# Optimization experiments

Hardware: AMD Instinct MI355X
Metric: run time of the kernel (lower is better)

Reference implementation:

```python
import jax, jax.numpy as jnp
import numpy as np

D_MODEL = 1024
EXPAND = 2
D_INNER = D_MODEL * EXPAND  # 2048
D_STATE = 16
FFN_HIDDEN = ((D_MODEL * 4 * 2 // 3) + 63) // 64 * 64  # 2752
EPS = 1e-6


def rmsnorm(x, w):
    return x * jax.lax.rsqrt(jnp.mean(x * x, axis=-1, keepdims=True) + EPS) * w


def selective_scan(z, dt_w, dt_b, x_proj_w, A_log, Dp):
    # z: [B, L, d_inner]
    dt = jax.nn.softplus(jnp.einsum('bld,ed->ble', z, dt_w) + dt_b)     # [B,L,d]
    BC = jnp.einsum('bld,nd->bln', z, x_proj_w)                          # [B,L,2n]
    Bm, Cm = BC[..., :D_STATE], BC[..., D_STATE:]                        # [B,L,n]
    A = -jnp.exp(A_log)                                                  # [d,n]
    dA = jnp.exp(dt[..., None] * A)                                      # [B,L,d,n]
    dBz = (dt * z)[..., None] * Bm[:, :, None, :]                        # [B,L,d,n]

    def combine(e1, e2):
        a1, b1 = e1
        a2, b2 = e2
        return (a1 * a2, a2 * b1 + b2)

    _, h = jax.lax.associative_scan(combine, (dA, dBz), axis=1)          # [B,L,d,n]
    y = jnp.einsum('bldn,bln->bld', h, Cm) + z * Dp
    return y


def setup_inputs() -> dict:
    key = jax.random.key(0)
    ks = jax.random.split(key, 12)
    s = 0.02
    inp = {
        'x': jax.random.normal(ks[0], (2, 1024, D_MODEL), dtype=jnp.float32),
        'norm1_w': jnp.ones((D_MODEL,), jnp.float32),
        'in_proj_w': jax.random.normal(ks[1], (D_INNER, D_MODEL), jnp.float32) * s,
        'gate_proj_w': jax.random.normal(ks[2], (D_INNER, D_MODEL), jnp.float32) * s,
        'dt_w': jax.random.normal(ks[3], (D_INNER, D_INNER), jnp.float32) * s,
        'dt_b': jnp.full((D_INNER,), -2.0, jnp.float32),
        'x_proj_w': jax.random.normal(ks[4], (2 * D_STATE, D_INNER), jnp.float32) * s,
        'A_log': jnp.broadcast_to(jnp.log(jnp.arange(1, D_STATE + 1, dtype=jnp.float32)), (D_INNER, D_STATE)).copy(),
        'Dp': jnp.ones((D_INNER,), jnp.float32),
        'out_proj_w': jax.random.normal(ks[5], (D_MODEL, D_INNER), jnp.float32) * s,
        'ffn_norm_w': jnp.ones((D_MODEL,), jnp.float32),
        'ffn_gate_w': jax.random.normal(ks[6], (FFN_HIDDEN, D_MODEL), jnp.float32) * s,
        'ffn_up_w': jax.random.normal(ks[7], (FFN_HIDDEN, D_MODEL), jnp.float32) * s,
        'ffn_down_w': jax.random.normal(ks[8], (D_MODEL, FFN_HIDDEN), jnp.float32) * s,
    }
    return inp


def reference(x, norm1_w, in_proj_w, gate_proj_w, dt_w, dt_b, x_proj_w, A_log, Dp,
              out_proj_w, ffn_norm_w, ffn_gate_w, ffn_up_w, ffn_down_w):
    residual = x
    h = rmsnorm(x, norm1_w)
    z = jnp.einsum('bld,ed->ble', h, in_proj_w)
    gate = jax.nn.sigmoid(jnp.einsum('bld,ed->ble', h, gate_proj_w))
    z = z * gate
    ssm_out = selective_scan(z, dt_w, dt_b, x_proj_w, A_log, Dp)
    x = residual + jnp.einsum('ble,de->bld', ssm_out, out_proj_w)
    hn = rmsnorm(x, ffn_norm_w)
    ff = jnp.einsum('blh,dh->bld',
                    jax.nn.silu(jnp.einsum('bld,hd->blh', hn, ffn_gate_w)) *
                    jnp.einsum('bld,hd->blh', hn, ffn_up_w),
                    ffn_down_w)
    return x + ff
```

## Files before the change

### kernel.cpp

```cpp
#include <hip/hip_runtime.h>
#include <cstdint>
#include <cstddef>


#define BM 128
#define BN 128
#define BK 32

typedef __attribute__((ext_vector_type(8))) short short8;
typedef __attribute__((ext_vector_type(4))) float floatx4;

__device__ __forceinline__ unsigned short f2bf(float f) {
  unsigned int u = __builtin_bit_cast(unsigned int, f);
  u = u + 0x7fffu + ((u >> 16) & 1u);
  return (unsigned short)(u >> 16);
}
__device__ __forceinline__ float bf2f(unsigned short u) {
  return __builtin_bit_cast(float, (unsigned int)u << 16);
}

__device__ __forceinline__ void async_copy16(const unsigned short* g, unsigned short* l) {
  __builtin_amdgcn_global_load_lds(
      (__attribute__((address_space(1))) void*)(const_cast<unsigned short*>(g)),
      (__attribute__((address_space(3))) void*)(l), 16, 0, 0);
}

struct CvtArgs {
  const float* src[8];
  unsigned short* dst[8];
  int rows[8];
  int cols4[8];
  int g0[9];
};

__global__ __launch_bounds__(256) void cvt_all(
    CvtArgs a, int nCvt,
    const float* __restrict__ x, const float* __restrict__ nw,
    unsigned short* __restrict__ h_bf) {
  __shared__ float ws_[4];
  if ((int)blockIdx.x >= nCvt) {
    int row = blockIdx.x - nCvt, t = threadIdx.x;
    float4 v = *(const float4*)&x[(size_t)row * 1024 + t * 4];
    float ss = v.x * v.x + v.y * v.y + v.z * v.z + v.w * v.w;
#pragma unroll
    for (int m = 1; m < 64; m <<= 1) ss += __shfl_xor(ss, m);
    if ((t & 63) == 0) ws_[t >> 6] = ss;
    __syncthreads();
    float tot = ws_[0] + ws_[1] + ws_[2] + ws_[3];
    float scale = rsqrtf(tot * (1.0f / 1024.0f) + 1e-6f);
    ushort4 o;
    o.x = f2bf(v.x * scale * nw[t * 4 + 0]);
    o.y = f2bf(v.y * scale * nw[t * 4 + 1]);
    o.z = f2bf(v.z * scale * nw[t * 4 + 2]);
    o.w = f2bf(v.w * scale * nw[t * 4 + 3]);
    *(ushort4*)&h_bf[(size_t)row * 1024 + t * 4] = o;
    return;
  }
  int i = blockIdx.x * 256 + threadIdx.x;
  if (i >= a.g0[8]) return;
  int s = 0;
#pragma unroll
  for (int k = 1; k < 8; ++k) s += (i >= a.g0[k]) ? 1 : 0;
  int li = i - a.g0[s];
  int cols4 = a.cols4[s];
  int r = li / cols4, c = li - r * cols4;
  ushort4 o = {0, 0, 0, 0};
  if (r < a.rows[s]) {
    float4 v = *(const float4*)&a.src[s][((size_t)r * cols4 + c) * 4];
    o.x = f2bf(v.x); o.y = f2bf(v.y); o.z = f2bf(v.z); o.w = f2bf(v.w);
  }
  *(ushort4*)&a.dst[s][((size_t)r * cols4 + c) * 4] = o;
}

__global__ __launch_bounds__(256) void rmsnorm_fuse3(
    const float* __restrict__ x, const float* __restrict__ p,
    const float* __restrict__ w,
    float* __restrict__ x2, unsigned short* __restrict__ outbf) {
  int row = blockIdx.x, t = threadIdx.x;
  size_t off = (size_t)row * 1024 + t * 4;
  float4 a = *(const float4*)&x[off];
  float4 b = *(const float4*)&p[off];
  float4 c = *(const float4*)&p[2097152ull + off];
  float4 d = *(const float4*)&p[4194304ull + off];
  float4 e = *(const float4*)&p[6291456ull + off];
  float4 v = {a.x + b.x + c.x + d.x + e.x, a.y + b.y + c.y + d.y + e.y,
              a.z + b.z + c.z + d.z + e.z, a.w + b.w + c.w + d.w + e.w};
  *(float4*)&x2[off] = v;
  float ss = v.x * v.x + v.y * v.y + v.z * v.z + v.w * v.w;
#pragma unroll
  for (int m = 1; m < 64; m <<= 1) ss += __shfl_xor(ss, m);
  __shared__ float ws_[4];
  if ((t & 63) == 0) ws_[t >> 6] = ss;
  __syncthreads();
  float tot = ws_[0] + ws_[1] + ws_[2] + ws_[3];
  float scale = rsqrtf(tot * (1.0f / 1024.0f) + 1e-6f);
  ushort4 o;
  o.x = f2bf(v.x * scale * w[t * 4 + 0]);
  o.y = f2bf(v.y * scale * w[t * 4 + 1]);
  o.z = f2bf(v.z * scale * w[t * 4 + 2]);
  o.w = f2bf(v.w * scale * w[t * 4 + 3]);
  *(ushort4*)&outbf[off] = o;
}

__global__ void final_add(const float* __restrict__ x2, const float* __restrict__ p,
                          float* __restrict__ out) {
  int i = blockIdx.x * 256 + threadIdx.x;
  float4 a = ((const float4*)x2)[i];
  float4 b = ((const float4*)p)[i];
  float4 c = ((const float4*)(p + 2097152ull))[i];
  float4 d = ((const float4*)(p + 4194304ull))[i];
  float4 e = ((const float4*)(p + 6291456ull))[i];
  float4 o = {a.x + b.x + c.x + d.x + e.x, a.y + b.y + c.y + d.y + e.y,
              a.z + b.z + c.z + d.z + e.z, a.w + b.w + c.w + d.w + e.w};
  ((float4*)out)[i] = o;
}

__global__ __launch_bounds__(256) void dtbc_red(
    const float* __restrict__ pd, const float* __restrict__ pb,
    const float* __restrict__ dtb, float* __restrict__ dt32,
    float* __restrict__ bc128) {
  int bi = blockIdx.x, t = threadIdx.x;
  if (bi < 4096) {
    int i = bi * 256 + t;
    int c4 = i & 511;
    size_t off = (size_t)i * 4;
    float4 a = *(const float4*)&pd[off];
    float4 b = *(const float4*)&pd[4194304ull + off];
    float4 g = *(const float4*)&dtb[c4 * 4];
    float4 v = {a.x + b.x + g.x, a.y + b.y + g.y, a.z + b.z + g.z, a.w + b.w + g.w};
    float4 o;
    o.x = fmaxf(v.x, 0.0f) + log1pf(__expf(-fabsf(v.x)));
    o.y = fmaxf(v.y, 0.0f) + log1pf(__expf(-fabsf(v.y)));
    o.z = fmaxf(v.z, 0.0f) + log1pf(__expf(-fabsf(v.z)));
    o.w = fmaxf(v.w, 0.0f) + log1pf(__expf(-fabsf(v.w)));
    *(float4*)&dt32[off] = o;
  } else {
    int i = (bi - 4096) * 256 + t;
    size_t off = (size_t)i * 4;
    float4 a = *(const float4*)&pb[off];
    float4 b = *(const float4*)&pb[262144ull + off];
    float4 o = {a.x + b.x, a.y + b.y, a.z + b.z, a.w + b.w};
    *(float4*)&bc128[off] = o;
  }
}

template <int EPI, int MAP>
__global__ __launch_bounds__(256, 4) void gemm_bt(
    const unsigned short* __restrict__ A,
    const unsigned short* __restrict__ W1,
    const unsigned short* __restrict__ W2,
    int n1_blocks, int ncols, int K,
    void* __restrict__ Cv, int ldc,
    float* __restrict__ C2) {
  __shared__ __align__(16) unsigned short As[2][BM * BK];
  __shared__ __align__(16) unsigned short Bs[2][BN * BK];
  int bn, bm, ks = 0, k0 = 0, nk;
  if (MAP == 0) {
    bn = blockIdx.x; bm = blockIdx.y;
    nk = K / BK;
  } else if (MAP == 2) {
    int l = blockIdx.x, i = l >> 3;
    bn = (l & 7) + 8 * (i % 6);
    bm = i / 6;
    if (bn >= ncols) return;
    nk = K / BK;
  } else if (MAP == 3) {
    bn = blockIdx.x & 7; bm = blockIdx.y;
    ks = blockIdx.x >> 3;
    int nkt = K / BK, base = nkt >> 2, rem = nkt & 3;
    nk = base + (ks < rem ? 1 : 0);
    int k0t = ks * base + (ks < rem ? ks : rem);
    k0 = k0t * BK;
  } else {
    if ((int)blockIdx.y < gridDim.y - 1) { bn = blockIdx.x; bm = blockIdx.y; }
    else                                 { bn = n1_blocks;  bm = blockIdx.x; }
    ks = blockIdx.z;
    k0 = ks * (K >> 1);
    nk = (K >> 1) / BK;
  }
  const int tid = threadIdx.x;
  const int wave = tid >> 6, lane = tid & 63;
  const unsigned short* W;
  int wrow0;
  if (bn < n1_blocks) { W = W1; wrow0 = bn * BN; }
  else                { W = W2; wrow0 = (bn - n1_blocks) * BN; }
  const int m0 = bm * BM;
  const int wm = wave >> 1, wn = wave & 1;
  const int l15 = lane & 15, quad = lane >> 4;

  floatx4 acc[4][4] = {};

  const int c0 = wave * 64 + lane;
  const int r0 = c0 >> 2, k0off = ((c0 & 3) ^ ((r0 >> 1) & 3)) * 8;
  const int c1 = c0 + 256;
  const int r1 = c1 >> 2, k1off = ((c1 & 3) ^ ((r1 >> 1) & 3)) * 8;

  auto stage = [&](int kb, int buf) {
    async_copy16(A + (size_t)(m0 + r0) * K + kb + k0off, &As[buf][c0 * 8]);
    async_copy16(A + (size_t)(m0 + r1) * K + kb + k1off, &As[buf][c1 * 8]);
    async_copy16(W + (size_t)(wrow0 + r0) * K + kb + k0off, &Bs[buf][c0 * 8]);
    async_copy16(W + (size_t)(wrow0 + r1) * K + kb + k1off, &Bs[buf][c1 * 8]);
  };

  stage(k0, 0);
  for (int kt = 0; kt < nk; ++kt) {
    const int cur = kt & 1;
    __syncthreads();
    if (kt + 1 < nk) stage(k0 + (kt + 1) * BK, cur ^ 1);

    short8 af[4], bf4[4];
#pragma unroll
    for (int i = 0; i < 4; ++i) {
      int row = wm * 64 + i * 16 + l15;
      af[i] = *(const short8*)&As[cur][(row * 4 + (quad ^ ((row >> 1) & 3))) * 8];
    }
#pragma unroll
    for (int j = 0; j < 4; ++j) {
      int row = wn * 64 + j * 16 + l15;
      bf4[j] = *(const short8*)&Bs[cur][(row * 4 + (quad ^ ((row >> 1) & 3))) * 8];
    }
#pragma unroll
    for (int i = 0; i < 4; ++i)
#pragma unroll
      for (int j = 0; j < 4; ++j)
        acc[i][j] = __builtin_amdgcn_mfma_f32_16x16x32_bf16(af[i], bf4[j], acc[i][j], 0, 0, 0);
  }

#pragma unroll
  for (int i = 0; i < 4; ++i)
#pragma unroll
    for (int j = 0; j < 4; ++j)
#pragma unroll
      for (int r = 0; r < 4; ++r) {
        int gr = m0 + wm * 64 + i * 16 + quad * 4 + r;
        int lc = wn * 64 + j * 16 + l15;
        int gc = bn * BN + lc;
        float v = acc[i][j][r];
        if (EPI == 0) {
          ((unsigned short*)Cv)[(size_t)gr * ldc + gc] = f2bf(v);
        } else if (EPI == 3) {
          ((float*)Cv)[(size_t)ks * 2097152 + (size_t)gr * ldc + gc] = v;
        } else {
          if (bn < n1_blocks)
            ((float*)Cv)[(size_t)ks * 4194304 + (size_t)gr * ldc + gc] = v;
          else
            C2[(size_t)ks * 262144 + (size_t)gr * 128 + lc] = v;
        }
      }
}

__global__ void zfuse(const unsigned short* __restrict__ zg, float* __restrict__ z32,
                      unsigned short* __restrict__ zbf) {
  int i = blockIdx.x * blockDim.x + threadIdx.x;
  int row = i >> 9, c4 = i & 511;
  ushort4 zr4 = *(const ushort4*)&zg[(size_t)row * 4096 + c4 * 4];
  ushort4 gr4 = *(const ushort4*)&zg[(size_t)row * 4096 + 2048 + c4 * 4];
  float4 o;
  o.x = bf2f(zr4.x) / (1.0f + __expf(-bf2f(gr4.x)));
  o.y = bf2f(zr4.y) / (1.0f + __expf(-bf2f(gr4.y)));
  o.z = bf2f(zr4.z) / (1.0f + __expf(-bf2f(gr4.z)));
  o.w = bf2f(zr4.w) / (1.0f + __expf(-bf2f(gr4.w)));
  *(float4*)&z32[(size_t)row * 2048 + c4 * 4] = o;
  ushort4 ob;
  ob.x = f2bf(o.x); ob.y = f2bf(o.y); ob.z = f2bf(o.z); ob.w = f2bf(o.w);
  *(ushort4*)&zbf[(size_t)row * 2048 + c4 * 4] = ob;
}

__device__ __forceinline__ void stage_bc(const float* __restrict__ bc128,
                                         int b, int c, float* bcs, int tid) {
  int row = tid >> 3, c4 = tid & 7;
  const float* src = bc128 + ((size_t)b * 1024 + c * 32 + row) * 128 + c4 * 4;
  *(float4*)&bcs[row * 32 + c4 * 4] = *(const float4*)src;
}

__global__ __launch_bounds__(256) void scan_phase1(
    const float* __restrict__ dt, const float* __restrict__ z,
    const float* __restrict__ bc128, const float* __restrict__ A_log,
    float* __restrict__ P, float* __restrict__ S) {
  const int d = blockIdx.x * 256 + threadIdx.x;
  const int c = blockIdx.y, b = blockIdx.z;
  __shared__ float bcs[1024];
  stage_bc(bc128, b, c, bcs, threadIdx.x);
  __syncthreads();
  float A2[16];
#pragma unroll
  for (int n = 0; n < 16; ++n) A2[n] = -__expf(A_log[d * 16 + n]) * 1.44269504f;
  float p[16], s[16];
#pragma unroll
  for (int n = 0; n < 16; ++n) { p[n] = 1.0f; s[n] = 0.0f; }
  const size_t base = ((size_t)b * 1024 + c * 32) * 2048 + d;
#pragma unroll 4
  for (int t = 0; t < 32; ++t) {
    float dtv = dt[base + (size_t)t * 2048];
    float zv  = z [base + (size_t)t * 2048];
    float dtz = dtv * zv;
#pragma unroll
    for (int n = 0; n < 16; ++n) {
      float dA = exp2f(dtv * A2[n]);
      s[n] = __builtin_fmaf(dA, s[n], dtz * bcs[t * 32 + n]);
      p[n] *= dA;
    }
  }
  float* Pp = P + (((size_t)c * 2 + b) * 2048 + d) * 16;
  float* Sp = S + (((size_t)c * 2 + b) * 2048 + d) * 16;
#pragma unroll
  for (int n = 0; n < 16; ++n) { Pp[n] = p[n]; Sp[n] = s[n]; }
}

__global__ __launch_bounds__(256) void scan_phase2(
    const float* __restrict__ P, const float* __restrict__ S,
    float* __restrict__ H) {
  int i = blockIdx.x * 256 + threadIdx.x;
  float h = 0.0f;
#pragma unroll
  for (int c = 0; c < 32; ++c) {
    size_t idx = (size_t)c * 65536 + i;
    H[idx] = h;
    h = __builtin_fmaf(P[idx], h, S[idx]);
  }
}

__global__ __launch_bounds__(256) void scan_phase3(
    const float* __restrict__ dt, const float* __restrict__ z,
    const float* __restrict__ bc128, const float* __restrict__ A_log,
    const float* __restrict__ Dp, const float* __restrict__ H,
    unsigned short* __restrict__ ybf) {
  const int d = blockIdx.x * 256 + threadIdx.x;
  const int c = blockIdx.y, b = blockIdx.z;
  __shared__ float bcs[1024];
  stage_bc(bc128, b, c, bcs, threadIdx.x);
  __syncthreads();
  float A2[16];
#pragma unroll
  for (int n = 0; n < 16; ++n) A2[n] = -__expf(A_log[d * 16 + n]) * 1.44269504f;
  float h[16];
  const float* Hp = H + (((size_t)c * 2 + b) * 2048 + d) * 16;
#pragma unroll
  for (int n = 0; n < 16; ++n) h[n] = Hp[n];
  const float Dd = Dp[d];
  const size_t base = ((size_t)b * 1024 + c * 32) * 2048 + d;
#pragma unroll 4
  for (int t = 0; t < 32; ++t) {
    float dtv = dt[base + (size_t)t * 2048];
    float zv  = z [base + (size_t)t * 2048];
    float dtz = dtv * zv;
    float y = zv * Dd;
#pragma unroll
    for (int n = 0; n < 16; ++n) {
      float dA = exp2f(dtv * A2[n]);
      h[n] = __builtin_fmaf(dA, h[n], dtz * bcs[t * 32 + n]);
      y = __builtin_fmaf(h[n], bcs[t * 32 + 16 + n], y);
    }
    ybf[base + (size_t)t * 2048] = f2bf(y);
  }
}

__global__ void actfuse(const unsigned short* __restrict__ gu,
                        unsigned short* __restrict__ act) {
  int i = blockIdx.x * blockDim.x + threadIdx.x;
  int row = i / 688, c4 = i - row * 688;
  ushort4 g4 = *(const ushort4*)&gu[(size_t)row * 5632 + c4 * 4];
  ushort4 u4 = *(const ushort4*)&gu[(size_t)row * 5632 + 2816 + c4 * 4];
  float gx = bf2f(g4.x), gy = bf2f(g4.y), gz = bf2f(g4.z), gw = bf2f(g4.w);
  ushort4 o;
  o.x = f2bf(gx / (1.0f + __expf(-gx)) * bf2f(u4.x));
  o.y = f2bf(gy / (1.0f + __expf(-gy)) * bf2f(u4.y));
  o.z = f2bf(gz / (1.0f + __expf(-gz)) * bf2f(u4.z));
  o.w = f2bf(gw / (1.0f + __expf(-gw)) * bf2f(u4.w));
  *(ushort4*)&act[(size_t)row * 2752 + c4 * 4] = o;
}

extern "C" void kernel_launch(void* const* d_in, const int* in_sizes, int n_in,
                              void* d_out, int out_size, void* d_ws, size_t ws_size,
                              hipStream_t stream) {
  const float* x         = (const float*)d_in[0];
  const float* norm1_w   = (const float*)d_in[1];
  const float* in_proj_w = (const float*)d_in[2];
  const float* gate_w    = (const float*)d_in[3];
  const float* dt_w      = (const float*)d_in[4];
  const float* dt_b      = (const float*)d_in[5];
  const float* x_proj_w  = (const float*)d_in[6];
  const float* A_log     = (const float*)d_in[7];
  const float* Dp        = (const float*)d_in[8];
  const float* out_w     = (const float*)d_in[9];
  const float* ffn_nw    = (const float*)d_in[10];
  const float* ffn_g     = (const float*)d_in[11];
  const float* ffn_u     = (const float*)d_in[12];
  const float* ffn_d     = (const float*)d_in[13];
  float* out = (float*)d_out;

  char* p = (char*)d_ws;
  auto alloc = [&](size_t b) { char* r = p; p += (b + 255) & ~(size_t)255; return r; };
  unsigned short* h_bf   = (unsigned short*)alloc(2048ull * 1024 * 2);
  float* big             = (float*)alloc(2048ull * 5632 * 4);
  float* pk              = (float*)alloc(4ull * 2048 * 1024 * 4);
  float* pkb             = (float*)alloc(2ull * 2048 * 128 * 4);
  float* z32             = (float*)alloc(2048ull * 2048 * 4);
  unsigned short* zbf    = (unsigned short*)alloc(2048ull * 2048 * 2);
  float* dt32            = (float*)alloc(2048ull * 2048 * 4);
  float* bc128           = (float*)alloc(2048ull * 128 * 4);
  unsigned short* ybf    = (unsigned short*)alloc(2048ull * 2048 * 2);
  float* x2              = (float*)alloc(2048ull * 1024 * 4);
  unsigned short* hn_bf  = (unsigned short*)alloc(2048ull * 1024 * 2);
  unsigned short* act_bf = (unsigned short*)alloc(2048ull * 2752 * 2);
  unsigned short* w_in   = (unsigned short*)alloc(2048ull * 1024 * 2);
  unsigned short* w_gate = (unsigned short*)alloc(2048ull * 1024 * 2);
  unsigned short* w_dt   = (unsigned short*)alloc(2048ull * 2048 * 2);
  unsigned short* w_xp   = (unsigned short*)alloc(128ull * 2048 * 2);
  unsigned short* w_out  = (unsigned short*)alloc(1024ull * 2048 * 2);
  unsigned short* w_g    = (unsigned short*)alloc(2816ull * 1024 * 2);
  unsigned short* w_u    = (unsigned short*)alloc(2816ull * 1024 * 2);
  unsigned short* w_d    = (unsigned short*)alloc(1024ull * 2752 * 2);

  unsigned short* zg_bf = (unsigned short*)big;
  unsigned short* gu_bf = (unsigned short*)big;
  float* pkd = big;
  float* Pb = big;
  float* Sb = big + 2097152;
  float* Hb = big + 4194304;

  CvtArgs ca;
  ca.src[0] = in_proj_w; ca.dst[0] = w_in;   ca.rows[0] = 2048; ca.cols4[0] = 256;
  ca.src[1] = gate_w;    ca.dst[1] = w_gate; ca.rows[1] = 2048; ca.cols4[1] = 256;
  ca.src[2] = dt_w;      ca.dst[2] = w_dt;   ca.rows[2] = 2048; ca.cols4[2] = 512;
  ca.src[3] = x_proj_w;  ca.dst[3] = w_xp;   ca.rows[3] = 32;   ca.cols4[3] = 512;
  ca.src[4] = out_w;     ca.dst[4] = w_out;  ca.rows[4] = 1024; ca.cols4[4] = 512;
  ca.src[5] = ffn_g;     ca.dst[5] = w_g;    ca.rows[5] = 2752; ca.cols4[5] = 256;
  ca.src[6] = ffn_u;     ca.dst[6] = w_u;    ca.rows[6] = 2752; ca.cols4[6] = 256;
  ca.src[7] = ffn_d;     ca.dst[7] = w_d;    ca.rows[7] = 1024; ca.cols4[7] = 688;
  int dstrows[8] = {2048, 2048, 2048, 128, 1024, 2816, 2816, 1024};
  int acc_g = 0;
  for (int s = 0; s < 8; ++s) { ca.g0[s] = acc_g; acc_g += dstrows[s] * ca.cols4[s]; }
  ca.g0[8] = acc_g;
  int nCvt = (acc_g + 255) / 256;
  cvt_all<<<nCvt + 2048, 256, 0, stream>>>(ca, nCvt, x, norm1_w, h_bf);

  gemm_bt<0, 0><<<dim3(32, 16), 256, 0, stream>>>(h_bf, w_in, w_gate, 16, 0, 1024, zg_bf, 4096, nullptr);
  zfuse<<<4096, 256, 0, stream>>>(zg_bf, z32, zbf);
  gemm_bt<4, 4><<<dim3(16, 17, 2), 256, 0, stream>>>(zbf, w_dt, w_xp, 16, 0, 2048, pkd, 2048, pkb);
  dtbc_red<<<4352, 256, 0, stream>>>(pkd, pkb, dt_b, dt32, bc128);
  scan_phase1<<<dim3(8, 32, 2), 256, 0, stream>>>(dt32, z32, bc128, A_log, Pb, Sb);
  scan_phase2<<<256, 256, 0, stream>>>(Pb, Sb, Hb);
  scan_phase3<<<dim3(8, 32, 2), 256, 0, stream>>>(dt32, z32, bc128, A_log, Dp, Hb, ybf);
  gemm_bt<3, 3><<<dim3(32, 16), 256, 0, stream>>>(ybf, w_out, w_out, 8, 0, 2048, pk, 1024, nullptr);
  rmsnorm_fuse3<<<2048, 256, 0, stream>>>(x, pk, ffn_nw, x2, hn_bf);
  gemm_bt<0, 2><<<768, 256, 0, stream>>>(hn_bf, w_g, w_u, 22, 44, 1024, gu_bf, 5632, nullptr);
  actfuse<<<5504, 256, 0, stream>>>(gu_bf, act_bf);
  gemm_bt<3, 3><<<dim3(32, 16), 256, 0, stream>>>(act_bf, w_d, w_d, 8, 0, 2752, pk, 1024, nullptr);
  final_add<<<2048, 256, 0, stream>>>(x2, pk, out);
}
```

Before: 396.8 us.

## Fuse gating and SwiGLU into GEMM epilogues via interleaved weights; fold dt reduction into scan

```diff
diff --git a/kernel.cpp b/kernel.cpp
--- a/kernel.cpp
+++ b/kernel.cpp
@@ -15,9 +15,6 @@
   u = u + 0x7fffu + ((u >> 16) & 1u);
   return (unsigned short)(u >> 16);
 }
-__device__ __forceinline__ float bf2f(unsigned short u) {
-  return __builtin_bit_cast(float, (unsigned int)u << 16);
-}
 
 __device__ __forceinline__ void async_copy16(const unsigned short* g, unsigned short* l) {
   __builtin_amdgcn_global_load_lds(
@@ -25,13 +22,8 @@
       (__attribute__((address_space(3))) void*)(l), 16, 0, 0);
 }
 
-struct CvtArgs {
-  const float* src[8];
-  unsigned short* dst[8];
-  int rows[8];
-  int cols4[8];
-  int g0[9];
-};
+struct Seg { const float* src; unsigned short* dst; int mode; int aux; };
+struct CvtArgs { Seg sg[10]; int g0[11]; };
 
 __global__ __launch_bounds__(256) void cvt_all(
     CvtArgs a, int nCvt,
@@ -57,19 +49,25 @@
     return;
   }
   int i = blockIdx.x * 256 + threadIdx.x;
-  if (i >= a.g0[8]) return;
+  if (i >= a.g0[10]) return;
   int s = 0;
 #pragma unroll
-  for (int k = 1; k < 8; ++k) s += (i >= a.g0[k]) ? 1 : 0;
+  for (int k = 1; k < 10; ++k) s += (i >= a.g0[k]) ? 1 : 0;
   int li = i - a.g0[s];
-  int cols4 = a.cols4[s];
-  int r = li / cols4, c = li - r * cols4;
-  ushort4 o = {0, 0, 0, 0};
-  if (r < a.rows[s]) {
-    float4 v = *(const float4*)&a.src[s][((size_t)r * cols4 + c) * 4];
-    o.x = f2bf(v.x); o.y = f2bf(v.y); o.z = f2bf(v.z); o.w = f2bf(v.w);
-  }
-  *(ushort4*)&a.dst[s][((size_t)r * cols4 + c) * 4] = o;
+  Seg sg = a.sg[s];
+  if (sg.mode == 2) {
+    ushort4 z = {0, 0, 0, 0};
+    *(ushort4*)&sg.dst[(size_t)li * 4] = z;
+  } else if (sg.mode == 0) {
+    float4 v = *(const float4*)&sg.src[(size_t)li * 4];
+    ushort4 o = {f2bf(v.x), f2bf(v.y), f2bf(v.z), f2bf(v.w)};
+    *(ushort4*)&sg.dst[(size_t)li * 4] = o;
+  } else {
+    int r = li >> 8, c = li & 255;
+    float4 v = *(const float4*)&sg.src[(size_t)li * 4];
+    ushort4 o = {f2bf(v.x), f2bf(v.y), f2bf(v.z), f2bf(v.w)};
+    *(ushort4*)&sg.dst[((size_t)(2 * r + sg.aux) * 256 + c) * 4] = o;
+  }
 }
 
 __global__ __launch_bounds__(256) void rmsnorm_fuse3(
@@ -113,35 +111,6 @@
   float4 o = {a.x + b.x + c.x + d.x + e.x, a.y + b.y + c.y + d.y + e.y,
               a.z + b.z + c.z + d.z + e.z, a.w + b.w + c.w + d.w + e.w};
   ((float4*)out)[i] = o;
-}
-
-__global__ __launch_bounds__(256) void dtbc_red(
-    const float* __restrict__ pd, const float* __restrict__ pb,
-    const float* __restrict__ dtb, float* __restrict__ dt32,
-    float* __restrict__ bc128) {
-  int bi = blockIdx.x, t = threadIdx.x;
-  if (bi < 4096) {
-    int i = bi * 256 + t;
-    int c4 = i & 511;
-    size_t off = (size_t)i * 4;
-    float4 a = *(const float4*)&pd[off];
-    float4 b = *(const float4*)&pd[4194304ull + off];
-    float4 g = *(const float4*)&dtb[c4 * 4];
-    float4 v = {a.x + b.x + g.x, a.y + b.y + g.y, a.z + b.z + g.z, a.w + b.w + g.w};
-    float4 o;
-    o.x = fmaxf(v.x, 0.0f) + log1pf(__expf(-fabsf(v.x)));
-    o.y = fmaxf(v.y, 0.0f) + log1pf(__expf(-fabsf(v.y)));
-    o.z = fmaxf(v.z, 0.0f) + log1pf(__expf(-fabsf(v.z)));
-    o.w = fmaxf(v.w, 0.0f) + log1pf(__expf(-fabsf(v.w)));
-    *(float4*)&dt32[off] = o;
-  } else {
-    int i = (bi - 4096) * 256 + t;
-    size_t off = (size_t)i * 4;
-    float4 a = *(const float4*)&pb[off];
-    float4 b = *(const float4*)&pb[262144ull + off];
-    float4 o = {a.x + b.x, a.y + b.y, a.z + b.z, a.w + b.w};
-    *(float4*)&bc128[off] = o;
-  }
 }
 
 template <int EPI, int MAP>
@@ -236,63 +205,71 @@
         int lc = wn * 64 + j * 16 + l15;
         int gc = bn * BN + lc;
         float v = acc[i][j][r];
-        if (EPI == 0) {
-          ((unsigned short*)Cv)[(size_t)gr * ldc + gc] = f2bf(v);
-        } else if (EPI == 3) {
+        if (EPI == 3) {
           ((float*)Cv)[(size_t)ks * 2097152 + (size_t)gr * ldc + gc] = v;
-        } else {
+        } else if (EPI == 4) {
           if (bn < n1_blocks)
             ((float*)Cv)[(size_t)ks * 4194304 + (size_t)gr * ldc + gc] = v;
           else
             C2[(size_t)ks * 262144 + (size_t)gr * 128 + lc] = v;
+        } else if (EPI == 5) {
+          float other = __shfl_xor(v, 1);
+          if (!(l15 & 1)) {
+            float zv = v / (1.0f + __expf(-other));
+            int f = gc >> 1;
+            ((float*)Cv)[(size_t)gr * 2048 + f] = zv;
+            ((unsigned short*)C2)[(size_t)gr * 2048 + f] = f2bf(zv);
+          }
+        } else {
+          float other = __shfl_xor(v, 1);
+          if (!(l15 & 1)) {
+            int f = gc >> 1;
+            if (f < 2752) {
+              float av = v / (1.0f + __expf(-v)) * other;
+              ((unsigned short*)Cv)[(size_t)gr * 2752 + f] = f2bf(av);
+            }
+          }
         }
       }
 }
 
-__global__ void zfuse(const unsigned short* __restrict__ zg, float* __restrict__ z32,
-                      unsigned short* __restrict__ zbf) {
-  int i = blockIdx.x * blockDim.x + threadIdx.x;
-  int row = i >> 9, c4 = i & 511;
-  ushort4 zr4 = *(const ushort4*)&zg[(size_t)row * 4096 + c4 * 4];
-  ushort4 gr4 = *(const ushort4*)&zg[(size_t)row * 4096 + 2048 + c4 * 4];
-  float4 o;
-  o.x = bf2f(zr4.x) / (1.0f + __expf(-bf2f(gr4.x)));
-  o.y = bf2f(zr4.y) / (1.0f + __expf(-bf2f(gr4.y)));
-  o.z = bf2f(zr4.z) / (1.0f + __expf(-bf2f(gr4.z)));
-  o.w = bf2f(zr4.w) / (1.0f + __expf(-bf2f(gr4.w)));
-  *(float4*)&z32[(size_t)row * 2048 + c4 * 4] = o;
-  ushort4 ob;
-  ob.x = f2bf(o.x); ob.y = f2bf(o.y); ob.z = f2bf(o.z); ob.w = f2bf(o.w);
-  *(ushort4*)&zbf[(size_t)row * 2048 + c4 * 4] = ob;
-}
-
-__device__ __forceinline__ void stage_bc(const float* __restrict__ bc128,
-                                         int b, int c, float* bcs, int tid) {
+__device__ __forceinline__ void stage_bc2(const float* __restrict__ pb,
+                                          int b, int c, float* bcs, int tid) {
   int row = tid >> 3, c4 = tid & 7;
-  const float* src = bc128 + ((size_t)b * 1024 + c * 32 + row) * 128 + c4 * 4;
-  *(float4*)&bcs[row * 32 + c4 * 4] = *(const float4*)src;
+  size_t idx = ((size_t)b * 1024 + c * 32 + row) * 128 + c4 * 4;
+  float4 aa = *(const float4*)&pb[idx];
+  float4 bb = *(const float4*)&pb[262144ull + idx];
+  float4 sm = {aa.x + bb.x, aa.y + bb.y, aa.z + bb.z, aa.w + bb.w};
+  *(float4*)&bcs[row * 32 + c4 * 4] = sm;
+}
+
+__device__ __forceinline__ float softplus_f(float v) {
+  return fmaxf(v, 0.0f) + log1pf(__expf(-fabsf(v)));
 }
 
 __global__ __launch_bounds__(256) void scan_phase1(
-    const float* __restrict__ dt, const float* __restrict__ z,
-    const float* __restrict__ bc128, const float* __restrict__ A_log,
+    const float* __restrict__ pd, const float* __restrict__ pb,
+    const float* __restrict__ dtb, const float* __restrict__ z,
+    const float* __restrict__ A_log,
     float* __restrict__ P, float* __restrict__ S) {
   const int d = blockIdx.x * 256 + threadIdx.x;
   const int c = blockIdx.y, b = blockIdx.z;
   __shared__ float bcs[1024];
-  stage_bc(bc128, b, c, bcs, threadIdx.x);
+  stage_bc2(pb, b, c, bcs, threadIdx.x);
   __syncthreads();
   float A2[16];
 #pragma unroll
   for (int n = 0; n < 16; ++n) A2[n] = -__expf(A_log[d * 16 + n]) * 1.44269504f;
+  const float bias = dtb[d];
   float p[16], s[16];
 #pragma unroll
   for (int n = 0; n < 16; ++n) { p[n] = 1.0f; s[n] = 0.0f; }
   const size_t base = ((size_t)b * 1024 + c * 32) * 2048 + d;
 #pragma unroll 4
   for (int t = 0; t < 32; ++t) {
-    float dtv = dt[base + (size_t)t * 2048];
-    float zv  = z [base + (size_t)t * 2048];
+    size_t off = base + (size_t)t * 2048;
+    float dtv = softplus_f(pd[off] + pd[4194304ull + off] + bias);
+    float zv  = z[off];
     float dtz = dtv * zv;
 #pragma unroll
     for (int n = 0; n < 16; ++n) {
@@ -321,18 +298,19 @@
 }
 
 __global__ __launch_bounds__(256) void scan_phase3(
-    const float* __restrict__ dt, const float* __restrict__ z,
-    const float* __restrict__ bc128, const float* __restrict__ A_log,
-    const float* __restrict__ Dp, const float* __restrict__ H,
-    unsigned short* __restrict__ ybf) {
+    const float* __restrict__ pd, const float* __restrict__ pb,
+    const float* __restrict__ dtb, const float* __restrict__ z,
+    const float* __restrict__ A_log, const float* __restrict__ Dp,
+    const float* __restrict__ H, unsigned short* __restrict__ ybf) {
   const int d = blockIdx.x * 256 + threadIdx.x;
   const int c = blockIdx.y, b = blockIdx.z;
   __shared__ float bcs[1024];
-  stage_bc(bc128, b, c, bcs, threadIdx.x);
+  stage_bc2(pb, b, c, bcs, threadIdx.x);
   __syncthreads();
   float A2[16];
 #pragma unroll
   for (int n = 0; n < 16; ++n) A2[n] = -__expf(A_log[d * 16 + n]) * 1.44269504f;
+  const float bias = dtb[d];
   float h[16];
   const float* Hp = H + (((size_t)c * 2 + b) * 2048 + d) * 16;
 #pragma unroll
@@ -341,8 +319,9 @@
   const size_t base = ((size_t)b * 1024 + c * 32) * 2048 + d;
 #pragma unroll 4
   for (int t = 0; t < 32; ++t) {
-    float dtv = dt[base + (size_t)t * 2048];
-    float zv  = z [base + (size_t)t * 2048];
+    size_t off = base + (size_t)t * 2048;
+    float dtv = softplus_f(pd[off] + pd[4194304ull + off] + bias);
+    float zv  = z[off];
     float dtz = dtv * zv;
     float y = zv * Dd;
 #pragma unroll
@@ -351,23 +330,8 @@
       h[n] = __builtin_fmaf(dA, h[n], dtz * bcs[t * 32 + n]);
       y = __builtin_fmaf(h[n], bcs[t * 32 + 16 + n], y);
     }
-    ybf[base + (size_t)t * 2048] = f2bf(y);
-  }
-}
-
-__global__ void actfuse(const unsigned short* __restrict__ gu,
-                        unsigned short* __restrict__ act) {
-  int i = blockIdx.x * blockDim.x + threadIdx.x;
-  int row = i / 688, c4 = i - row * 688;
-  ushort4 g4 = *(const ushort4*)&gu[(size_t)row * 5632 + c4 * 4];
-  ushort4 u4 = *(const ushort4*)&gu[(size_t)row * 5632 + 2816 + c4 * 4];
-  float gx = bf2f(g4.x), gy = bf2f(g4.y), gz = bf2f(g4.z), gw = bf2f(g4.w);
-  ushort4 o;
-  o.x = f2bf(gx / (1.0f + __expf(-gx)) * bf2f(u4.x));
-  o.y = f2bf(gy / (1.0f + __expf(-gy)) * bf2f(u4.y));
-  o.z = f2bf(gz / (1.0f + __expf(-gz)) * bf2f(u4.z));
-  o.w = f2bf(gw / (1.0f + __expf(-gw)) * bf2f(u4.w));
-  *(ushort4*)&act[(size_t)row * 2752 + c4 * 4] = o;
+    ybf[off] = f2bf(y);
+  }
 }
 
 extern "C" void kernel_launch(void* const* d_in, const int* in_sizes, int n_in,
@@ -397,55 +361,52 @@
   float* pkb             = (float*)alloc(2ull * 2048 * 128 * 4);
   float* z32             = (float*)alloc(2048ull * 2048 * 4);
   unsigned short* zbf    = (unsigned short*)alloc(2048ull * 2048 * 2);
-  float* dt32            = (float*)alloc(2048ull * 2048 * 4);
-  float* bc128           = (float*)alloc(2048ull * 128 * 4);
   unsigned short* ybf    = (unsigned short*)alloc(2048ull * 2048 * 2);
   float* x2              = (float*)alloc(2048ull * 1024 * 4);
   unsigned short* hn_bf  = (unsigned short*)alloc(2048ull * 1024 * 2);
   unsigned short* act_bf = (unsigned short*)alloc(2048ull * 2752 * 2);
-  unsigned short* w_in   = (unsigned short*)alloc(2048ull * 1024 * 2);
-  unsigned short* w_gate = (unsigned short*)alloc(2048ull * 1024 * 2);
+  unsigned short* w_zg   = (unsigned short*)alloc(4096ull * 1024 * 2);
   unsigned short* w_dt   = (unsigned short*)alloc(2048ull * 2048 * 2);
   unsigned short* w_xp   = (unsigned short*)alloc(128ull * 2048 * 2);
   unsigned short* w_out  = (unsigned short*)alloc(1024ull * 2048 * 2);
-  unsigned short* w_g    = (unsigned short*)alloc(2816ull * 1024 * 2);
-  unsigned short* w_u    = (unsigned short*)alloc(2816ull * 1024 * 2);
+  unsigned short* w_gu   = (unsigned short*)alloc(5632ull * 1024 * 2);
   unsigned short* w_d    = (unsigned short*)alloc(1024ull * 2752 * 2);
 
-  unsigned short* zg_bf = (unsigned short*)big;
-  unsigned short* gu_bf = (unsigned short*)big;
   float* pkd = big;
-  float* Pb = big;
-  float* Sb = big + 2097152;
-  float* Hb = big + 4194304;
+  float* Pb = pk;
+  float* Sb = pk + 2097152;
+  float* Hb = pk + 4194304;
 
   CvtArgs ca;
-  ca.src[0] = in_proj_w; ca.dst[0] = w_in;   ca.rows[0] = 2048; ca.cols4[0] = 256;
-  ca.src[1] = gate_w;    ca.dst[1] = w_gate; ca.rows[1] = 2048; ca.cols4[1] = 256;
-  ca.src[2] = dt_w;      ca.dst[2] = w_dt;   ca.rows[2] = 2048; ca.cols4[2] = 512;
-  ca.src[3] = x_proj_w;  ca.dst[3] = w_xp;   ca.rows[3] = 32;   ca.cols4[3] = 512;
-  ca.src[4] = out_w;     ca.dst[4] = w_out;  ca.rows[4] = 1024; ca.cols4[4] = 512;
-  ca.src[5] = ffn_g;     ca.dst[5] = w_g;    ca.rows[5] = 2752; ca.cols4[5] = 256;
-  ca.src[6] = ffn_u;     ca.dst[6] = w_u;    ca.rows[6] = 2752; ca.cols4[6] = 256;
-  ca.src[7] = ffn_d;     ca.dst[7] = w_d;    ca.rows[7] = 1024; ca.cols4[7] = 688;
-  int dstrows[8] = {2048, 2048, 2048, 128, 1024, 2816, 2816, 1024};
+  auto seg = [&](int idx, const float* s, unsigned short* d, int mode, int aux, int groups,
+                 int& acc_g) {
+    ca.sg[idx] = {s, d, mode, aux};
+    ca.g0[idx] = acc_g;
+    acc_g += groups;
+  };
   int acc_g = 0;
-  for (int s = 0; s < 8; ++s) { ca.g0[s] = acc_g; acc_g += dstrows[s] * ca.cols4[s]; }
-  ca.g0[8] = acc_g;
+  seg(0, in_proj_w, w_zg,                 1, 0, 2048 * 256, acc_g);
+  seg(1, gate_w,    w_zg,                 1, 1, 2048 * 256, acc_g);
+  seg(2, dt_w,      w_dt,                 0, 0, 2048 * 512, acc_g);
+  seg(3, x_proj_w,  w_xp,                 0, 0, 32 * 512,   acc_g);
+  seg(4, nullptr,   w_xp + 32ull * 2048,  2, 0, 96 * 512,   acc_g);
+  seg(5, out_w,     w_out,                0, 0, 1024 * 512, acc_g);
+  seg(6, ffn_g,     w_gu,                 1, 0, 2752 * 256, acc_g);
+  seg(7, ffn_u,     w_gu,                 1, 1, 2752 * 256, acc_g);
+  seg(8, nullptr,   w_gu + 5504ull * 1024, 2, 0, 128 * 256, acc_g);
+  seg(9, ffn_d,     w_d,                  0, 0, 1024 * 688, acc_g);
+  ca.g0[10] = acc_g;
   int nCvt = (acc_g + 255) / 256;
   cvt_all<<<nCvt + 2048, 256, 0, stream>>>(ca, nCvt, x, norm1_w, h_bf);
 
-  gemm_bt<0, 0><<<dim3(32, 16), 256, 0, stream>>>(h_bf, w_in, w_gate, 16, 0, 1024, zg_bf, 4096, nullptr);
-  zfuse<<<4096, 256, 0, stream>>>(zg_bf, z32, zbf);
+  gemm_bt<5, 0><<<dim3(32, 16), 256, 0, stream>>>(h_bf, w_zg, w_zg, 32, 0, 1024, z32, 2048, (float*)zbf);
   gemm_bt<4, 4><<<dim3(16, 17, 2), 256, 0, stream>>>(zbf, w_dt, w_xp, 16, 0, 2048, pkd, 2048, pkb);
-  dtbc_red<<<4352, 256, 0, stream>>>(pkd, pkb, dt_b, dt32, bc128);
-  scan_phase1<<<dim3(8, 32, 2), 256, 0, stream>>>(dt32, z32, bc128, A_log, Pb, Sb);
+  scan_phase1<<<dim3(8, 32, 2), 256, 0, stream>>>(pkd, pkb, dt_b, z32, A_log, Pb, Sb);
   scan_phase2<<<256, 256, 0, stream>>>(Pb, Sb, Hb);
-  scan_phase3<<<dim3(8, 32, 2), 256, 0, stream>>>(dt32, z32, bc128, A_log, Dp, Hb, ybf);
+  scan_phase3<<<dim3(8, 32, 2), 256, 0, stream>>>(pkd, pkb, dt_b, z32, A_log, Dp, Hb, ybf);
   gemm_bt<3, 3><<<dim3(32, 16), 256, 0, stream>>>(ybf, w_out, w_out, 8, 0, 2048, pk, 1024, nullptr);
   rmsnorm_fuse3<<<2048, 256, 0, stream>>>(x, pk, ffn_nw, x2, hn_bf);
-  gemm_bt<0, 2><<<768, 256, 0, stream>>>(hn_bf, w_g, w_u, 22, 44, 1024, gu_bf, 5632, nullptr);
-  actfuse<<<5504, 256, 0, stream>>>(gu_bf, act_bf);
+  gemm_bt<6, 2><<<768, 256, 0, stream>>>(hn_bf, w_gu, w_gu, 44, 44, 1024, act_bf, 2752, nullptr);
   gemm_bt<3, 3><<<dim3(32, 16), 256, 0, stream>>>(act_bf, w_d, w_d, 8, 0, 2752, pk, 1024, nullptr);
   final_add<<<2048, 256, 0, stream>>>(x2, pk, out);
 }
```

Result: no change. 400.7 us (+1.0%).
